# Kernel optimization log

Measured on AMD Instinct MI355X. Metric: run time of the kernel, lower is better.

Reference implementation:

```python
import jax, jax.numpy as jnp
import numpy as np

DIM = 1024
NH = 16
HD = DIM // NH  # 64
WS = 14         # window size
DFF = 4 * DIM
EPS = 1e-6


def layernorm(x, scale, bias):
    m = jnp.mean(x, axis=-1, keepdims=True)
    v = jnp.var(x, axis=-1, keepdims=True)
    return (x - m) * jax.lax.rsqrt(v + EPS) * scale + bias


def get_rel_pos(q_size, k_size, rel_pos):
    # table size (2*WS-1, HD) matches max_rel_dist, so no resize needed
    coords = (jnp.arange(q_size)[:, None] - jnp.arange(k_size)[None, :] + (k_size - 1)).astype(jnp.int32)
    return rel_pos[coords.reshape(-1)].reshape(q_size, k_size, -1)  # (q,k,HD)


def window_partition(x):
    b, h, w, c = x.shape
    pad_h = (WS - h % WS) % WS
    pad_w = (WS - w % WS) % WS
    # faithful to source: pad_w applied on axis 1, pad_h on axis 2
    x = jnp.pad(x, ((0, 0), (0, pad_w), (0, pad_h), (0, 0)))
    hp, wp = h + pad_h, w + pad_w
    x = x.reshape(b, hp // WS, WS, wp // WS, WS, c)
    windows = x.transpose(0, 1, 3, 2, 4, 5).reshape(-1, WS, WS, c)
    return windows, (hp, wp)


def window_unpartition(windows, pad_hw, hw):
    hp, wp = pad_hw
    h, w = hw
    b = windows.shape[0] // (hp * wp // WS // WS)
    x = windows.reshape(b, hp // WS, wp // WS, WS, WS, -1)
    x = x.transpose(0, 1, 3, 2, 4, 5).reshape(b, hp, wp, -1)
    return x[:, :h, :w, :]


def attention(x, qkv_kernel, qkv_bias, rel_pos_h, rel_pos_w, proj_kernel, proj_bias):
    b, h, w, _ = x.shape
    qkv = x @ qkv_kernel + qkv_bias                                  # (b,h,w,3*DIM)
    qkv = qkv.reshape(b, h * w, 3, NH, HD).transpose(2, 0, 3, 1, 4)
    qkv = qkv.reshape(3, b * NH, h * w, HD)
    q, k, v = qkv[0], qkv[1], qkv[2]
    attn = (q * HD ** -0.5) @ k.transpose(0, 2, 1)                   # (b*NH, hw, hw)
    rh = get_rel_pos(h, h, rel_pos_h)                                # (h,h,HD)
    rw = get_rel_pos(w, w, rel_pos_w)                                # (w,w,HD)
    r_q = q.reshape(-1, h, w, HD)
    rel_h = jnp.einsum('bhwc,hkc->bhwk', r_q, rh)
    rel_w = jnp.einsum('bhwc,wkc->bhwk', r_q, rw)
    attn = (attn.reshape(-1, h, w, h, w) + rel_h[:, :, :, :, None] + rel_w[:, :, :, None, :]).reshape(-1, h * w, h * w)
    attn = jax.nn.softmax(attn, axis=-1)
    out = (attn @ v).reshape(b, NH, h, w, HD).transpose(0, 2, 3, 1, 4).reshape(b, h, w, DIM)
    return out @ proj_kernel + proj_bias


def setup_inputs() -> dict:
    key = jax.random.key(0)
    ks = jax.random.split(key, 8)
    s = 0.02
    B, H, W = 4, 64, 64
    return {
        'x': jax.random.normal(ks[0], (B, H, W, DIM), jnp.float32),
        'norm1_scale': jnp.ones((DIM,), jnp.float32),
        'norm1_bias': jnp.zeros((DIM,), jnp.float32),
        'qkv_kernel': jax.random.normal(ks[1], (DIM, 3 * DIM), jnp.float32) * s,
        'qkv_bias': jnp.zeros((3 * DIM,), jnp.float32),
        'rel_pos_h': jax.random.normal(ks[2], (2 * WS - 1, HD), jnp.float32) * s,
        'rel_pos_w': jax.random.normal(ks[3], (2 * WS - 1, HD), jnp.float32) * s,
        'proj_kernel': jax.random.normal(ks[4], (DIM, DIM), jnp.float32) * s,
        'proj_bias': jnp.zeros((DIM,), jnp.float32),
        'norm2_scale': jnp.ones((DIM,), jnp.float32),
        'norm2_bias': jnp.zeros((DIM,), jnp.float32),
        'fc1_kernel': jax.random.normal(ks[5], (DIM, DFF), jnp.float32) * s,
        'fc1_bias': jnp.zeros((DFF,), jnp.float32),
        'fc2_kernel': jax.random.normal(ks[6], (DFF, DIM), jnp.float32) * s,
        'fc2_bias': jnp.zeros((DIM,), jnp.float32),
    }


def reference(x, norm1_scale, norm1_bias, qkv_kernel, qkv_bias, rel_pos_h, rel_pos_w,
              proj_kernel, proj_bias, norm2_scale, norm2_bias,
              fc1_kernel, fc1_bias, fc2_kernel, fc2_bias):
    shortcut = x
    h, w = x.shape[1], x.shape[2]
    y = layernorm(x, norm1_scale, norm1_bias)
    y, pad_hw = window_partition(y)
    y = attention(y, qkv_kernel, qkv_bias, rel_pos_h, rel_pos_w, proj_kernel, proj_bias)
    y = window_unpartition(y, pad_hw, (h, w))
    x = shortcut + y                           # drop_path=0, no layer scale
    z = layernorm(x, norm2_scale, norm2_bias)
    z = jax.nn.gelu(z @ fc1_kernel + fc1_bias, approximate=False)
    z = z @ fc2_kernel + fc2_bias
    return x + z
```

## Files before the change

kernel.cpp:

```cpp
#include <hip/hip_runtime.h>

typedef __attribute__((ext_vector_type(8))) short bf16x8;
typedef __attribute__((ext_vector_type(4))) float f32x4;
typedef __attribute__((ext_vector_type(16))) float f32x16;

__device__ __forceinline__ float b2f(ushort u) {
    union { unsigned int i; float f; } v; v.i = ((unsigned int)u) << 16; return v.f;
}
__device__ __forceinline__ ushort f2b(float f) {
    union { float f; unsigned int i; } v; v.f = f;
    unsigned int i = v.i;
    return (ushort)((i + 0x7FFFu + ((i >> 16) & 1u)) >> 16);
}
__device__ __forceinline__ void glds16(const ushort* g, ushort* l) {
    __builtin_amdgcn_global_load_lds((const __attribute__((address_space(1))) void*)g,
                                     (__attribute__((address_space(3))) void*)l, 16, 0, 0);
}
__device__ __forceinline__ void BARX() {
    asm volatile("" ::: "memory");
    __builtin_amdgcn_s_barrier();
    asm volatile("" ::: "memory");
}

__global__ __launch_bounds__(256) void ln_kernel(const float* __restrict__ x,
                                                 const float* __restrict__ sc,
                                                 const float* __restrict__ bi,
                                                 ushort* __restrict__ y) {
    __shared__ float red[8];
    long row = blockIdx.x;
    const float* xr = x + row * 1024;
    int t = threadIdx.x;
    float4 u = *(const float4*)(xr + t * 4);
    float s = u.x + u.y + u.z + u.w;
    float q = u.x * u.x + u.y * u.y + u.z * u.z + u.w * u.w;
    for (int off = 32; off > 0; off >>= 1) {
        s += __shfl_xor(s, off);
        q += __shfl_xor(q, off);
    }
    if ((t & 63) == 0) { red[t >> 6] = s; red[4 + (t >> 6)] = q; }
    __syncthreads();
    s = red[0] + red[1] + red[2] + red[3];
    q = red[4] + red[5] + red[6] + red[7];
    float mean = s * (1.0f / 1024.0f);
    float var = q * (1.0f / 1024.0f) - mean * mean;
    float rstd = rsqrtf(fmaxf(var, 0.0f) + 1e-6f);
    int c = t * 4;
    float o0 = (u.x - mean) * rstd * sc[c + 0] + bi[c + 0];
    float o1 = (u.y - mean) * rstd * sc[c + 1] + bi[c + 1];
    float o2 = (u.z - mean) * rstd * sc[c + 2] + bi[c + 2];
    float o3 = (u.w - mean) * rstd * sc[c + 3] + bi[c + 3];
    uint2 o;
    o.x = (unsigned int)f2b(o0) | ((unsigned int)f2b(o1) << 16);
    o.y = (unsigned int)f2b(o2) | ((unsigned int)f2b(o3) << 16);
    *(uint2*)(y + row * 1024 + c) = o;
}

__global__ __launch_bounds__(256) void ln_part_kernel(const float* __restrict__ x,
                                                      const float* __restrict__ sc,
                                                      const float* __restrict__ bi,
                                                      ushort* __restrict__ wy,
                                                      int win_base, int nvalid) {
    __shared__ float red[8];
    int wt = blockIdx.x;
    int lwin = wt / 196, rr = wt % 196;
    int t = threadIdx.x;
    int valid = 0;
    long xrow = 0;
    if (lwin < nvalid) {
        int gwin = win_base + lwin;
        int img = gwin / 25, wrem = gwin % 25;
        int gh = (wrem / 5) * 14 + rr / 14;
        int gw = (wrem % 5) * 14 + rr % 14;
        if (gh < 64 && gw < 64) {
            valid = 1;
            xrow = (long)img * 4096 + gh * 64 + gw;
        }
    }
    uint2 o; o.x = 0u; o.y = 0u;
    if (valid) {
        const float* xr = x + xrow * 1024;
        float4 u = *(const float4*)(xr + t * 4);
        float s = u.x + u.y + u.z + u.w;
        float q = u.x * u.x + u.y * u.y + u.z * u.z + u.w * u.w;
        for (int off = 32; off > 0; off >>= 1) {
            s += __shfl_xor(s, off);
            q += __shfl_xor(q, off);
        }
        if ((t & 63) == 0) { red[t >> 6] = s; red[4 + (t >> 6)] = q; }
        __syncthreads();
        s = red[0] + red[1] + red[2] + red[3];
        q = red[4] + red[5] + red[6] + red[7];
        float mean = s * (1.0f / 1024.0f);
        float var = q * (1.0f / 1024.0f) - mean * mean;
        float rstd = rsqrtf(fmaxf(var, 0.0f) + 1e-6f);
        int c = t * 4;
        float o0 = (u.x - mean) * rstd * sc[c + 0] + bi[c + 0];
        float o1 = (u.y - mean) * rstd * sc[c + 1] + bi[c + 1];
        float o2 = (u.z - mean) * rstd * sc[c + 2] + bi[c + 2];
        float o3 = (u.w - mean) * rstd * sc[c + 3] + bi[c + 3];
        o.x = (unsigned int)f2b(o0) | ((unsigned int)f2b(o1) << 16);
        o.y = (unsigned int)f2b(o2) | ((unsigned int)f2b(o3) << 16);
    }
    *(uint2*)(wy + (long)wt * 1024 + t * 4) = o;
}

__global__ void transpose_w(const float* __restrict__ in, ushort* __restrict__ out,
                            int K, int N) {
    __shared__ float tile[32][33];
    int n0 = blockIdx.x * 32, k0 = blockIdx.y * 32;
    int tx = threadIdx.x, ty = threadIdx.y;
    for (int i = 0; i < 32; i += 8)
        tile[ty + i][tx] = in[(long)(k0 + ty + i) * N + n0 + tx];
    __syncthreads();
    for (int i = 0; i < 32; i += 8)
        out[(long)(n0 + ty + i) * K + k0 + tx] = f2b(tile[tx][ty + i]);
}

template <int FLAGS, typename OT>
__global__ __launch_bounds__(256) void gemm_bt(const ushort* __restrict__ A,
                                               const ushort* __restrict__ Bt,
                                               const float* __restrict__ bias,
                                               const float* __restrict__ resid,
                                               OT* __restrict__ out,
                                               int M, int N, int K) {
    __shared__ __align__(16) ushort As[128 * 32];
    __shared__ __align__(16) ushort Bs[128 * 32];
    const int tid = threadIdx.x;
    const int lane = tid & 63, w = tid >> 6;
    const int wm = (w >> 1) * 64, wn = (w & 1) * 64;
    const int quad = lane >> 4, l16 = lane & 15;
    const int bm = blockIdx.x * 128, bn = blockIdx.y * 128;
    const int r = tid >> 2, kc = (tid & 3) * 8;
    f32x4 acc[4][4];
#pragma unroll
    for (int i = 0; i < 4; i++)
#pragma unroll
        for (int j = 0; j < 4; j++) acc[i][j] = (f32x4){0.f, 0.f, 0.f, 0.f};
    const ushort* Ag = A + (long)(bm + r) * K + kc;
    const ushort* Bg = Bt + (long)(bn + r) * K + kc;
    ushort* AsW = As + w * 512;
    ushort* BsW = Bs + w * 512;
    for (int k0 = 0; k0 < K; k0 += 32) {
        __syncthreads();
        glds16(Ag + k0, AsW);
        glds16(Ag + (long)64 * K + k0, AsW + 2048);
        glds16(Bg + k0, BsW);
        glds16(Bg + (long)64 * K + k0, BsW + 2048);
        __syncthreads();
        bf16x8 afr[4], bfr[4];
#pragma unroll
        for (int t = 0; t < 4; t++) {
            afr[t] = *(const bf16x8*)&As[(wm + t * 16 + l16) * 32 + quad * 8];
            bfr[t] = *(const bf16x8*)&Bs[(wn + t * 16 + l16) * 32 + quad * 8];
        }
#pragma unroll
        for (int tm = 0; tm < 4; tm++)
#pragma unroll
            for (int tn = 0; tn < 4; tn++)
                acc[tm][tn] = __builtin_amdgcn_mfma_f32_16x16x32_bf16(afr[tm], bfr[tn],
                                                                     acc[tm][tn], 0, 0, 0);
    }
#pragma unroll
    for (int tm = 0; tm < 4; tm++) {
#pragma unroll
        for (int j = 0; j < 4; j++) {
            int gm = bm + wm + tm * 16 + quad * 4 + j;
#pragma unroll
            for (int tn = 0; tn < 4; tn++) {
                int gn = bn + wn + tn * 16 + l16;
                float v = acc[tm][tn][j] + bias[gn];
                if (FLAGS & 1) v = 0.5f * v * (1.0f + erff(v * 0.70710678118654752f));
                if (FLAGS & 2) v += resid[(long)gm * N + gn];
                if (sizeof(OT) == 4) out[(long)gm * N + gn] = (OT)v;
                else out[(long)gm * N + gn] = (OT)f2b(v);
            }
        }
    }
}

#define DSR(dst, addr, imm) \
    asm volatile("ds_read_b128 %0, %1 offset:%2" : "=&v"(dst) : "v"(addr), "n"(imm));

#define MFMA32(mf, nf, a, b) \
    acc[mf][nf] = __builtin_amdgcn_mfma_f32_32x32x16_bf16(a, b, acc[mf][nf], 0, 0, 0);

#define RDK0(buf) \
    DSR(y0, b_k0, (buf) * 16384 + 0)    DSR(y1, b_k0, (buf) * 16384 + 2048) \
    DSR(x0, a_k0, (buf) * 16384 + 0)    DSR(x1, a_k0, (buf) * 16384 + 2048) \
    DSR(x2, a_k0, (buf) * 16384 + 4096) DSR(x3, a_k0, (buf) * 16384 + 6144)

#define RDK1(buf) \
    DSR(Y0, b_k1, (buf) * 16384 + 0)    DSR(Y1, b_k1, (buf) * 16384 + 2048) \
    DSR(X0, a_k1, (buf) * 16384 + 0)    DSR(X1, a_k1, (buf) * 16384 + 2048) \
    DSR(X2, a_k1, (buf) * 16384 + 4096) DSR(X3, a_k1, (buf) * 16384 + 6144)

#define MFK0 \
    MFMA32(0, 0, x0, y0) MFMA32(0, 1, x0, y1) MFMA32(1, 0, x1, y0) MFMA32(1, 1, x1, y1) \
    MFMA32(2, 0, x2, y0) MFMA32(2, 1, x2, y1) MFMA32(3, 0, x3, y0) MFMA32(3, 1, x3, y1)

#define MFK1 \
    MFMA32(0, 0, X0, Y0) MFMA32(0, 1, X0, Y1) MFMA32(1, 0, X1, Y0) MFMA32(1, 1, X1, Y1) \
    MFMA32(2, 0, X2, Y0) MFMA32(2, 1, X2, Y1) MFMA32(3, 0, X3, Y0) MFMA32(3, 1, X3, Y1)

#define LGW6 asm volatile("s_waitcnt lgkmcnt(6)" ::: "memory"); \
    __builtin_amdgcn_sched_barrier(0);

#define STAGE4(ts, dbuf) \
    glds16(Ag + (long)(ts) * 32, &As[dbuf][sdst]); \
    glds16(Ag2 + (long)(ts) * 32, &As[dbuf][sdst + 4096]); \
    glds16(Bg + (long)(ts) * 32, &Bs[dbuf][sdst]); \
    glds16(Bg2 + (long)(ts) * 32, &Bs[dbuf][sdst + 4096]);

#define TILEF(bb, ts) do {                                                               \
    STAGE4(ts + 3, ((bb) + 3) & 3)                                                       \
    __builtin_amdgcn_sched_barrier(0);                                                   \
    asm volatile("s_waitcnt vmcnt(4)" ::: "memory");                                     \
    RDK1(bb)                                                                             \
    LGW6                                                                                 \
    __builtin_amdgcn_s_setprio(1);                                                       \
    MFK0                                                                                 \
    __builtin_amdgcn_s_setprio(0);                                                       \
    __builtin_amdgcn_sched_barrier(0);                                                   \
    RDK0(((bb) + 1) & 3)                                                                 \
    LGW6                                                                                 \
    __builtin_amdgcn_s_setprio(1);                                                       \
    MFK1                                                                                 \
    __builtin_amdgcn_s_setprio(0);                                                       \
    __builtin_amdgcn_sched_barrier(0);                                                   \
    BARX();                                                                              \
} while (0)

template <int FLAGS, typename OT>
__global__ __launch_bounds__(512, 2) void gemm256(const ushort* __restrict__ A,
                                                  const ushort* __restrict__ Bt,
                                                  const float* __restrict__ bias,
                                                  const float* __restrict__ resid,
                                                  OT* __restrict__ out,
                                                  int M, int N, int K, int nbn) {
    __shared__ __align__(64) ushort As[4][8192];
    __shared__ __align__(64) ushort Bs[4][8192];
    const int nwg = gridDim.x;
    const int orig = blockIdx.x;
    const int q8 = nwg >> 3, r8 = nwg & 7;
    const int xcd = orig & 7, sub = orig >> 3;
    const int wgid = (xcd < r8 ? xcd * (q8 + 1) : r8 * (q8 + 1) + (xcd - r8) * q8) + sub;
    const int bm = (wgid / nbn) * 256, bn = (wgid % nbn) * 256;

    const int tid = threadIdx.x;
    const int lane = tid & 63, w = tid >> 6;
    const int l31 = lane & 31, hi = lane >> 5;
    const int wm = (w >> 2) * 128, wn = (w & 3) * 64;

    const int r_st = w * 16 + (lane >> 2);
    const int c_st = (((lane & 3) ^ ((lane >> 2) & 3) ^ ((lane >> 4) & 1)) << 3);
    const ushort* Ag = A + (long)(bm + r_st) * K + c_st;
    const ushort* Ag2 = Ag + (long)128 * K;
    const ushort* Bg = Bt + (long)(bn + r_st) * K + c_st;
    const ushort* Bg2 = Bg + (long)128 * K;
    const int sdst = w * 512;

    const int swz = (lane & 3) ^ ((lane >> 2) & 1);
    const int s0 = swz & 1, s1 = swz >> 1;
    const int slot_k0 = (((0 ^ s1) << 1) | (hi ^ s0)) << 4;
    const int slot_k1 = (((1 ^ s1) << 1) | (hi ^ s0)) << 4;
    const unsigned As0 =
        (unsigned)(size_t)(__attribute__((address_space(3))) ushort*)&As[0][0];
    const unsigned Bs0 =
        (unsigned)(size_t)(__attribute__((address_space(3))) ushort*)&Bs[0][0];
    const unsigned a_k0 = As0 + (unsigned)((wm + l31) * 64 + slot_k0);
    const unsigned a_k1 = As0 + (unsigned)((wm + l31) * 64 + slot_k1);
    const unsigned b_k0 = Bs0 + (unsigned)((wn + l31) * 64 + slot_k0);
    const unsigned b_k1 = Bs0 + (unsigned)((wn + l31) * 64 + slot_k1);

    f32x16 acc[4][2];
#pragma unroll
    for (int i = 0; i < 4; i++)
#pragma unroll
        for (int j = 0; j < 2; j++)
#pragma unroll
            for (int e = 0; e < 16; e++) acc[i][j][e] = 0.f;

    bf16x8 x0, x1, x2, x3, y0, y1;
    bf16x8 X0, X1, X2, X3, Y0, Y1;

    glds16(Ag, &As[0][sdst]);       glds16(Ag2, &As[0][sdst + 4096]);
    glds16(Bg, &Bs[0][sdst]);       glds16(Bg2, &Bs[0][sdst + 4096]);
    glds16(Ag + 32, &As[1][sdst]);  glds16(Ag2 + 32, &As[1][sdst + 4096]);
    glds16(Bg + 32, &Bs[1][sdst]);  glds16(Bg2 + 32, &Bs[1][sdst + 4096]);
    glds16(Ag + 64, &As[2][sdst]);  glds16(Ag2 + 64, &As[2][sdst + 4096]);
    glds16(Bg + 64, &Bs[2][sdst]);  glds16(Bg2 + 64, &Bs[2][sdst + 4096]);
    __builtin_amdgcn_sched_barrier(0);
    asm volatile("s_waitcnt vmcnt(4)" ::: "memory");
    BARX();
    RDK0(0)

    const int nt = K >> 5;
    for (int t = 0; t + 8 <= nt; t += 4) {
        TILEF(0, t);
        TILEF(1, t + 1);
        TILEF(2, t + 2);
        TILEF(3, t + 3);
    }
    TILEF(0, nt - 4);
    RDK1(1)
    LGW6
    __builtin_amdgcn_s_setprio(1); MFK0 __builtin_amdgcn_s_setprio(0);
    __builtin_amdgcn_sched_barrier(0);
    RDK0(2)
    LGW6
    __builtin_amdgcn_s_setprio(1); MFK1 __builtin_amdgcn_s_setprio(0);
    __builtin_amdgcn_sched_barrier(0);
    asm volatile("s_waitcnt vmcnt(0)" ::: "memory");
    BARX();
    RDK1(2)
    LGW6
    __builtin_amdgcn_s_setprio(1); MFK0 __builtin_amdgcn_s_setprio(0);
    __builtin_amdgcn_sched_barrier(0);
    RDK0(3)
    LGW6
    __builtin_amdgcn_s_setprio(1); MFK1 __builtin_amdgcn_s_setprio(0);
    __builtin_amdgcn_sched_barrier(0);
    RDK1(3)
    LGW6
    __builtin_amdgcn_s_setprio(1); MFK0 __builtin_amdgcn_s_setprio(0);
    __builtin_amdgcn_sched_barrier(0);
    asm volatile("s_waitcnt lgkmcnt(0)" ::: "memory");
    __builtin_amdgcn_sched_barrier(0);
    __builtin_amdgcn_s_setprio(1); MFK1 __builtin_amdgcn_s_setprio(0);
    __builtin_amdgcn_sched_barrier(0);

#pragma unroll
    for (int mf = 0; mf < 4; mf++) {
#pragma unroll
        for (int nf = 0; nf < 2; nf++) {
            const int gn = bn + wn + nf * 32 + l31;
#pragma unroll
            for (int q = 0; q < 4; q++) {
#pragma unroll
                for (int j = 0; j < 4; j++) {
                    const int gm = bm + wm + mf * 32 + q * 8 + j + 4 * hi;
                    const long ro = (long)gm * N;
                    float v = acc[mf][nf][q * 4 + j] + bias[gn];
                    if (FLAGS & 1) v = 0.5f * v * (1.0f + erff(v * 0.70710678118654752f));
                    if (FLAGS & 2) v += resid[ro + gn];
                    if (sizeof(OT) == 4) out[ro + gn] = (OT)v;
                    else out[ro + gn] = (OT)f2b(v);
                }
            }
        }
    }
}

__global__ __launch_bounds__(256) void attn_kernel(const ushort* __restrict__ qkv,
                                                   ushort* __restrict__ o_out,
                                                   const float* __restrict__ relH,
                                                   const float* __restrict__ relW,
                                                   int win0, long orow0) {
    __shared__ __align__(16) ushort Vt[64 * 200];
    __shared__ __align__(16) ushort Ps[64 * 104];
    __shared__ __align__(16) ushort sc[8 * 448];
    const int head = blockIdx.y;
    const long qbase = (long)blockIdx.x * 196 * 3072 + head * 64;
    const int gwin = win0 + blockIdx.x;
    const int img = gwin / 25, wrem = gwin % 25;
    const int whh = (wrem / 5) * 14, www = (wrem % 5) * 14;
    const int tid = threadIdx.x, lane = tid & 63, w = tid >> 6;
    const int quad = lane >> 4, l16 = lane & 15;

    for (int idx = tid; idx < 196 * 64; idx += 256) {
        int k = idx >> 6, d = idx & 63;
        Vt[d * 200 + k] = qkv[qbase + 2048 + (long)k * 3072 + d];
    }
    __syncthreads();

    bf16x8 bH[2][2], bW[2][2];
#pragma unroll
    for (int nt = 0; nt < 2; nt++) {
        int n = nt * 16 + l16;
#pragma unroll
        for (int kt = 0; kt < 2; kt++) {
            bf16x8 rh = (bf16x8){0, 0, 0, 0, 0, 0, 0, 0};
            bf16x8 rw = (bf16x8){0, 0, 0, 0, 0, 0, 0, 0};
            if (n < 27) {
                const float* ph = relH + n * 64 + kt * 32 + quad * 8;
                const float* pw = relW + n * 64 + kt * 32 + quad * 8;
#pragma unroll
                for (int e = 0; e < 8; e++) {
                    rh[e] = (short)f2b(ph[e]);
                    rw[e] = (short)f2b(pw[e]);
                }
            }
            bH[nt][kt] = rh;
            bW[nt][kt] = rw;
        }
    }

    for (int tr = w; tr < 13; tr += 4) {
        int qrow = tr * 16 + l16;
        if (qrow > 195) qrow = 195;
        bf16x8 qf0 = *(const bf16x8*)(qkv + qbase + (long)qrow * 3072 + quad * 8);
        bf16x8 qf1 = *(const bf16x8*)(qkv + qbase + (long)qrow * 3072 + 32 + quad * 8);

#pragma unroll
        for (int tab = 0; tab < 2; tab++) {
#pragma unroll
            for (int nt = 0; nt < 2; nt++) {
                f32x4 a = (f32x4){0.f, 0.f, 0.f, 0.f};
                a = __builtin_amdgcn_mfma_f32_16x16x32_bf16(qf0, tab ? bW[nt][0] : bH[nt][0],
                                                            a, 0, 0, 0);
                a = __builtin_amdgcn_mfma_f32_16x16x32_bf16(qf1, tab ? bW[nt][1] : bH[nt][1],
                                                            a, 0, 0, 0);
                int col = nt * 16 + l16;
                if (col < 27) {
#pragma unroll
                    for (int j = 0; j < 4; j++)
                        sc[(w * 2 + tab) * 448 + (quad * 4 + j) * 28 + col] = f2b(a[j]);
                }
            }
        }

        f32x4 sf[13];
#pragma unroll
        for (int tc = 0; tc < 13; tc++) {
            int krow = tc * 16 + l16;
            if (krow > 195) krow = 195;
            const ushort* kp = qkv + qbase + 1024 + (long)krow * 3072 + quad * 8;
            bf16x8 kf0 = *(const bf16x8*)kp;
            bf16x8 kf1 = *(const bf16x8*)(kp + 32);
            f32x4 s = (f32x4){0.f, 0.f, 0.f, 0.f};
            s = __builtin_amdgcn_mfma_f32_16x16x32_bf16(qf0, kf0, s, 0, 0, 0);
            s = __builtin_amdgcn_mfma_f32_16x16x32_bf16(qf1, kf1, s, 0, 0, 0);
            sf[tc] = s;
        }
#pragma unroll
        for (int tc = 0; tc < 13; tc++) {
            int c = tc * 16 + l16;
            if (c < 196) {
                int kh = c / 14, kw = c - kh * 14;
#pragma unroll
                for (int j = 0; j < 4; j++) {
                    int rr = tr * 16 + quad * 4 + j;
                    if (rr > 195) rr = 195;
                    float dh = b2f(sc[(w * 2 + 0) * 448 + (quad * 4 + j) * 28 +
                                      (rr / 14 - kh + 13)]);
                    float dw = b2f(sc[(w * 2 + 1) * 448 + (quad * 4 + j) * 28 +
                                      (rr % 14 - kw + 13)]);
                    sf[tc][j] = sf[tc][j] * 0.125f + dh + dw;
                }
            } else {
#pragma unroll
                for (int j = 0; j < 4; j++) sf[tc][j] = -30000.0f;
            }
        }
        f32x4 mx = sf[0];
#pragma unroll
        for (int tc = 1; tc < 13; tc++)
#pragma unroll
            for (int j = 0; j < 4; j++) mx[j] = fmaxf(mx[j], sf[tc][j]);
        for (int off = 1; off < 16; off <<= 1)
#pragma unroll
            for (int j = 0; j < 4; j++) mx[j] = fmaxf(mx[j], __shfl_xor(mx[j], off));
        f32x4 sum = (f32x4){0.f, 0.f, 0.f, 0.f};
#pragma unroll
        for (int tc = 0; tc < 13; tc++)
#pragma unroll
            for (int j = 0; j < 4; j++) {
                float p = __expf(sf[tc][j] - mx[j]);
                sf[tc][j] = p;
                sum[j] += p;
            }
        for (int off = 1; off < 16; off <<= 1)
#pragma unroll
            for (int j = 0; j < 4; j++) sum[j] += __shfl_xor(sum[j], off);
        f32x4 linv;
#pragma unroll
        for (int j = 0; j < 4; j++) linv[j] = 1.0f / sum[j];

        f32x4 oa[4];
#pragma unroll
        for (int tn = 0; tn < 4; tn++) oa[tn] = (f32x4){0.f, 0.f, 0.f, 0.f};
#pragma unroll
        for (int tc = 0; tc < 6; tc++) {
            int c = tc * 16 + l16;
#pragma unroll
            for (int j = 0; j < 4; j++)
                Ps[(w * 16 + quad * 4 + j) * 104 + c] = f2b(sf[tc][j]);
        }
#pragma unroll
        for (int ks = 0; ks < 3; ks++) {
            bf16x8 pf = *(const bf16x8*)&Ps[(w * 16 + l16) * 104 + ks * 32 + quad * 8];
#pragma unroll
            for (int tn = 0; tn < 4; tn++) {
                bf16x8 vf = *(const bf16x8*)&Vt[(tn * 16 + l16) * 200 + ks * 32 + quad * 8];
                oa[tn] = __builtin_amdgcn_mfma_f32_16x16x32_bf16(pf, vf, oa[tn], 0, 0, 0);
            }
        }
#pragma unroll
        for (int tc = 6; tc < 13; tc++) {
            int c = tc * 16 + l16;
            if (c < 196) {
#pragma unroll
                for (int j = 0; j < 4; j++)
                    Ps[(w * 16 + quad * 4 + j) * 104 + (c - 96)] = f2b(sf[tc][j]);
            }
        }
#pragma unroll
        for (int ks = 0; ks < 3; ks++) {
            bf16x8 pf = *(const bf16x8*)&Ps[(w * 16 + l16) * 104 + ks * 32 + quad * 8];
#pragma unroll
            for (int tn = 0; tn < 4; tn++) {
                bf16x8 vf = *(const bf16x8*)&Vt[(tn * 16 + l16) * 200 + 96 + ks * 32 + quad * 8];
                oa[tn] = __builtin_amdgcn_mfma_f32_16x16x32_bf16(pf, vf, oa[tn], 0, 0, 0);
            }
        }
        for (int kk = 192; kk < 196; kk++) {
            float pj[4];
#pragma unroll
            for (int j = 0; j < 4; j++)
                pj[j] = b2f(Ps[(w * 16 + quad * 4 + j) * 104 + 96 + (kk - 192)]);
#pragma unroll
            for (int tn = 0; tn < 4; tn++) {
                float vv = b2f(Vt[(tn * 16 + l16) * 200 + kk]);
#pragma unroll
                for (int j = 0; j < 4; j++) oa[tn][j] += pj[j] * vv;
            }
        }
#pragma unroll
        for (int j = 0; j < 4; j++) {
            int rr = tr * 16 + quad * 4 + j;
            if (rr < 196) {
                int gh = whh + rr / 14, gw = www + rr % 14;
                if (gh < 64 && gw < 64) {
                    long orow = (long)img * 4096 + gh * 64 + gw - orow0;
#pragma unroll
                    for (int tn = 0; tn < 4; tn++)
                        o_out[orow * 1024 + head * 64 + tn * 16 + l16] =
                            f2b(oa[tn][j] * linv[j]);
                }
            }
        }
    }
}

extern "C" void kernel_launch(void* const* d_in, const int* in_sizes, int n_in,
                              void* d_out, int out_size, void* d_ws, size_t ws_size,
                              hipStream_t stream) {
    const float* x = (const float*)d_in[0];
    const float* n1s = (const float*)d_in[1];
    const float* n1b = (const float*)d_in[2];
    const float* qkvW = (const float*)d_in[3];
    const float* qkvB = (const float*)d_in[4];
    const float* relH = (const float*)d_in[5];
    const float* relW = (const float*)d_in[6];
    const float* projW = (const float*)d_in[7];
    const float* projB = (const float*)d_in[8];
    const float* n2s = (const float*)d_in[9];
    const float* n2b = (const float*)d_in[10];
    const float* fc1W = (const float*)d_in[11];
    const float* fc1B = (const float*)d_in[12];
    const float* fc2W = (const float*)d_in[13];
    const float* fc2B = (const float*)d_in[14];
    float* OUT = (float*)d_out;
    char* ws = (char*)d_ws;

    if (ws_size >= 221000000ULL) {
        ushort* T0  = (ushort*)(ws);
        ushort* TP  = (ushort*)(ws + 6291456ULL);
        ushort* TF1 = (ushort*)(ws + 8388608ULL);
        ushort* TF2 = (ushort*)(ws + 16777216ULL);
        ushort* W0  = (ushort*)(ws + 25165824ULL);
        ushort* QKV = (ushort*)(ws + 65536000ULL);
        ushort* AO  = (ushort*)(ws + 186646528ULL);
        ushort* Z   = (ushort*)(ws + 25165824ULL);
        ushort* H   = (ushort*)(ws + 58720256ULL);

        transpose_w<<<dim3(96, 32), dim3(32, 8), 0, stream>>>(qkvW, T0, 1024, 3072);
        transpose_w<<<dim3(32, 32), dim3(32, 8), 0, stream>>>(projW, TP, 1024, 1024);
        transpose_w<<<dim3(128, 32), dim3(32, 8), 0, stream>>>(fc1W, TF1, 1024, 4096);
        transpose_w<<<dim3(32, 128), dim3(32, 8), 0, stream>>>(fc2W, TF2, 4096, 1024);
        ln_part_kernel<<<19712, 256, 0, stream>>>(x, n1s, n1b, W0, 0, 100);
        gemm256<0, ushort><<<924, 512, 0, stream>>>(W0, T0, qkvB, nullptr, QKV,
                                                    19712, 3072, 1024, 12);
        attn_kernel<<<dim3(100, 16), 256, 0, stream>>>(QKV, AO, relH, relW, 0, 0L);
        gemm256<2, float><<<256, 512, 0, stream>>>(AO, TP, projB, x, OUT,
                                                   16384, 1024, 1024, 4);
        ln_kernel<<<16384, 256, 0, stream>>>(OUT, n2s, n2b, Z);
        gemm256<1, ushort><<<1024, 512, 0, stream>>>(Z, TF1, fc1B, nullptr, H,
                                                     16384, 4096, 1024, 16);
        gemm256<2, float><<<256, 512, 0, stream>>>(H, TF2, fc2B, OUT, OUT,
                                                   16384, 1024, 4096, 4);
    } else if (ws_size >= 100000000ULL) {
        ushort* T0  = (ushort*)(ws);
        ushort* TP  = (ushort*)(ws + 6291456ULL);
        ushort* TF1 = (ushort*)(ws + 8388608ULL);
        ushort* TF2 = (ushort*)(ws + 16777216ULL);
        ushort* AO  = (ushort*)(ws + 25165824ULL);
        ushort* W0  = (ushort*)(ws + 58720256ULL);
        ushort* QKV = (ushort*)(ws + 68943872ULL);
        ushort* Z   = (ushort*)(ws + 25165824ULL);
        ushort* H   = (ushort*)(ws + 58720256ULL);

        transpose_w<<<dim3(96, 32), dim3(32, 8), 0, stream>>>(qkvW, T0, 1024, 3072);
        transpose_w<<<dim3(32, 32), dim3(32, 8), 0, stream>>>(projW, TP, 1024, 1024);
        transpose_w<<<dim3(128, 32), dim3(32, 8), 0, stream>>>(fc1W, TF1, 1024, 4096);
        transpose_w<<<dim3(32, 128), dim3(32, 8), 0, stream>>>(fc2W, TF2, 4096, 1024);
        for (int i = 0; i < 4; i++) {
            ln_part_kernel<<<4992, 256, 0, stream>>>(x, n1s, n1b, W0, i * 25, 25);
            gemm_bt<0, ushort><<<dim3(39, 24), 256, 0, stream>>>(W0, T0, qkvB, nullptr,
                                                                 QKV, 4992, 3072, 1024);
            attn_kernel<<<dim3(25, 16), 256, 0, stream>>>(QKV, AO, relH, relW, i * 25, 0L);
        }
        gemm_bt<2, float><<<dim3(128, 8), 256, 0, stream>>>(AO, TP, projB, x, OUT,
                                                            16384, 1024, 1024);
        for (int c = 0; c < 4; c++) {
            float* xc = OUT + (long)c * 4194304;
            ln_kernel<<<4096, 256, 0, stream>>>(xc, n2s, n2b, Z);
            gemm_bt<1, ushort><<<dim3(32, 32), 256, 0, stream>>>(Z, TF1, fc1B, nullptr, H,
                                                                 4096, 4096, 1024);
            gemm_bt<2, float><<<dim3(32, 8), 256, 0, stream>>>(H, TF2, fc2B, xc, xc,
                                                               4096, 1024, 4096);
        }
    } else {
        ushort* T0 = (ushort*)(ws);
        ushort* W0 = (ushort*)(ws + 6291456ULL);
        ushort* W1 = (ushort*)(ws + 16515072ULL);
        ushort* W2 = (ushort*)(ws + 22806528ULL);
        ushort* F1 = (ushort*)(ws);
        ushort* F2 = (ushort*)(ws + 8388608ULL);
        ushort* Z  = (ushort*)(ws + 16777216ULL);
        ushort* H  = (ushort*)(ws + 18874368ULL);

        transpose_w<<<dim3(96, 32), dim3(32, 8), 0, stream>>>(qkvW, T0, 1024, 3072);
        for (int i = 0; i < 4; i++) {
            const float* xi = x + (long)i * 4194304;
            ln_part_kernel<<<4992, 256, 0, stream>>>(x, n1s, n1b, W0, i * 25, 25);
            for (int g = 0; g < 5; g++) {
                gemm_bt<0, ushort><<<dim3(8, 24), 256, 0, stream>>>(
                    W0 + (long)g * 980 * 1024, T0, qkvB, nullptr, W1, 1024, 3072, 1024);
                attn_kernel<<<dim3(5, 16), 256, 0, stream>>>(W1, W2, relH, relW,
                                                             i * 25 + g * 5, (long)i * 4096);
            }
            transpose_w<<<dim3(32, 32), dim3(32, 8), 0, stream>>>(projW, W1, 1024, 1024);
            gemm_bt<2, float><<<dim3(32, 8), 256, 0, stream>>>(
                W2, W1, projB, xi, OUT + (long)i * 4194304, 4096, 1024, 1024);
        }
        transpose_w<<<dim3(128, 32), dim3(32, 8), 0, stream>>>(fc1W, F1, 1024, 4096);
        transpose_w<<<dim3(32, 128), dim3(32, 8), 0, stream>>>(fc2W, F2, 4096, 1024);
        for (int c = 0; c < 16; c++) {
            float* xc = OUT + (long)c * 1048576;
            ln_kernel<<<1024, 256, 0, stream>>>(xc, n2s, n2b, Z);
            gemm_bt<1, ushort><<<dim3(8, 32), 256, 0, stream>>>(Z, F1, fc1B, nullptr, H,
                                                                1024, 4096, 1024);
            gemm_bt<2, float><<<dim3(8, 8), 256, 0, stream>>>(H, F2, fc2B, xc, xc,
                                                              1024, 1024, 4096);
        }
    }
}
```

Before: 909.3 us.

## Load GEMM A operand directly from global into registers, staging only B in LDS

The 256x256 bf16 GEMM kernel stops staging the A tile through shared memory. Each wave now loads its own A fragments straight from global memory into double-buffered registers one k-step ahead, while B stays in a 4-stage LDS ring, now filled with a different per-wave row mapping. This halves LDS traffic and capacity per block and removes the A ds_reads. In exchange it raises VGPR pressure, and because the two waves sharing an M half both read the same A rows, global and L2 traffic for A doubles, with less latency hiding for those loads.

```diff
diff --git a/kernel.cpp b/kernel.cpp
--- a/kernel.cpp
+++ b/kernel.cpp
@@ -185,46 +185,51 @@
     acc[mf][nf] = __builtin_amdgcn_mfma_f32_32x32x16_bf16(a, b, acc[mf][nf], 0, 0, 0);
 
 #define RDK0(buf) \
-    DSR(y0, b_k0, (buf) * 16384 + 0)    DSR(y1, b_k0, (buf) * 16384 + 2048) \
-    DSR(x0, a_k0, (buf) * 16384 + 0)    DSR(x1, a_k0, (buf) * 16384 + 2048) \
-    DSR(x2, a_k0, (buf) * 16384 + 4096) DSR(x3, a_k0, (buf) * 16384 + 6144)
-
+    DSR(y0, b_k0, (buf) * 16384 + 0)    DSR(y1, b_k0, (buf) * 16384 + 2048)
 #define RDK1(buf) \
-    DSR(Y0, b_k1, (buf) * 16384 + 0)    DSR(Y1, b_k1, (buf) * 16384 + 2048) \
-    DSR(X0, a_k1, (buf) * 16384 + 0)    DSR(X1, a_k1, (buf) * 16384 + 2048) \
-    DSR(X2, a_k1, (buf) * 16384 + 4096) DSR(X3, a_k1, (buf) * 16384 + 6144)
-
-#define MFK0 \
-    MFMA32(0, 0, x0, y0) MFMA32(0, 1, x0, y1) MFMA32(1, 0, x1, y0) MFMA32(1, 1, x1, y1) \
-    MFMA32(2, 0, x2, y0) MFMA32(2, 1, x2, y1) MFMA32(3, 0, x3, y0) MFMA32(3, 1, x3, y1)
-
-#define MFK1 \
-    MFMA32(0, 0, X0, Y0) MFMA32(0, 1, X0, Y1) MFMA32(1, 0, X1, Y0) MFMA32(1, 1, X1, Y1) \
-    MFMA32(2, 0, X2, Y0) MFMA32(2, 1, X2, Y1) MFMA32(3, 0, X3, Y0) MFMA32(3, 1, X3, Y1)
-
-#define LGW6 asm volatile("s_waitcnt lgkmcnt(6)" ::: "memory"); \
-    __builtin_amdgcn_sched_barrier(0);
-
-#define STAGE4(ts, dbuf) \
-    glds16(Ag + (long)(ts) * 32, &As[dbuf][sdst]); \
-    glds16(Ag2 + (long)(ts) * 32, &As[dbuf][sdst + 4096]); \
-    glds16(Bg + (long)(ts) * 32, &Bs[dbuf][sdst]); \
-    glds16(Bg2 + (long)(ts) * 32, &Bs[dbuf][sdst + 4096]);
-
-#define TILEF(bb, ts) do {                                                               \
-    STAGE4(ts + 3, ((bb) + 3) & 3)                                                       \
+    DSR(Y0, b_k1, (buf) * 16384 + 0)    DSR(Y1, b_k1, (buf) * 16384 + 2048)
+
+#define MFK0(S) \
+    MFMA32(0, 0, S##0, y0) MFMA32(0, 1, S##0, y1) MFMA32(1, 0, S##1, y0) MFMA32(1, 1, S##1, y1) \
+    MFMA32(2, 0, S##2, y0) MFMA32(2, 1, S##2, y1) MFMA32(3, 0, S##3, y0) MFMA32(3, 1, S##3, y1)
+#define MFK1(S) \
+    MFMA32(0, 0, S##4, Y0) MFMA32(0, 1, S##4, Y1) MFMA32(1, 0, S##5, Y0) MFMA32(1, 1, S##5, Y1) \
+    MFMA32(2, 0, S##6, Y0) MFMA32(2, 1, S##6, Y1) MFMA32(3, 0, S##7, Y0) MFMA32(3, 1, S##7, Y1)
+
+#define LGW2 asm volatile("s_waitcnt lgkmcnt(2)" ::: "memory"); \
+    __builtin_amdgcn_sched_barrier(0);
+#define LGW0 asm volatile("s_waitcnt lgkmcnt(0)" ::: "memory"); \
+    __builtin_amdgcn_sched_barrier(0);
+
+#define ALOAD(S, ts) \
+    S##0 = *(const bf16x8*)(Ar0 + (ts) * 32);      \
+    S##1 = *(const bf16x8*)(Ar1 + (ts) * 32);      \
+    S##2 = *(const bf16x8*)(Ar2 + (ts) * 32);      \
+    S##3 = *(const bf16x8*)(Ar3 + (ts) * 32);      \
+    S##4 = *(const bf16x8*)(Ar0 + (ts) * 32 + 16); \
+    S##5 = *(const bf16x8*)(Ar1 + (ts) * 32 + 16); \
+    S##6 = *(const bf16x8*)(Ar2 + (ts) * 32 + 16); \
+    S##7 = *(const bf16x8*)(Ar3 + (ts) * 32 + 16);
+
+#define STAGE_B(ts, dbuf) \
+    glds16(Bg0 + (long)(ts) * 32, &Bs[dbuf][w * 1024]); \
+    glds16(Bg1 + (long)(ts) * 32, &Bs[dbuf][w * 1024 + 512]);
+
+#define TILEX(bb, ts, CUR, NXT) do {                                                     \
+    STAGE_B(ts + 3, ((bb) + 3) & 3)                                                      \
+    ALOAD(NXT, ts + 1)                                                                   \
     __builtin_amdgcn_sched_barrier(0);                                                   \
-    asm volatile("s_waitcnt vmcnt(4)" ::: "memory");                                     \
+    asm volatile("s_waitcnt vmcnt(10)" ::: "memory");                                    \
     RDK1(bb)                                                                             \
-    LGW6                                                                                 \
+    LGW2                                                                                 \
     __builtin_amdgcn_s_setprio(1);                                                       \
-    MFK0                                                                                 \
+    MFK0(CUR)                                                                            \
     __builtin_amdgcn_s_setprio(0);                                                       \
     __builtin_amdgcn_sched_barrier(0);                                                   \
     RDK0(((bb) + 1) & 3)                                                                 \
-    LGW6                                                                                 \
+    LGW2                                                                                 \
     __builtin_amdgcn_s_setprio(1);                                                       \
-    MFK1                                                                                 \
+    MFK1(CUR)                                                                            \
     __builtin_amdgcn_s_setprio(0);                                                       \
     __builtin_amdgcn_sched_barrier(0);                                                   \
     BARX();                                                                              \
@@ -237,7 +242,6 @@
                                                   const float* __restrict__ resid,
                                                   OT* __restrict__ out,
                                                   int M, int N, int K, int nbn) {
-    __shared__ __align__(64) ushort As[4][8192];
     __shared__ __align__(64) ushort Bs[4][8192];
     const int nwg = gridDim.x;
     const int orig = blockIdx.x;
@@ -251,24 +255,21 @@
     const int l31 = lane & 31, hi = lane >> 5;
     const int wm = (w >> 2) * 128, wn = (w & 3) * 64;
 
-    const int r_st = w * 16 + (lane >> 2);
     const int c_st = (((lane & 3) ^ ((lane >> 2) & 3) ^ ((lane >> 4) & 1)) << 3);
-    const ushort* Ag = A + (long)(bm + r_st) * K + c_st;
-    const ushort* Ag2 = Ag + (long)128 * K;
-    const ushort* Bg = Bt + (long)(bn + r_st) * K + c_st;
-    const ushort* Bg2 = Bg + (long)128 * K;
-    const int sdst = w * 512;
+    const ushort* Bg0 = Bt + (long)(bn + w * 32 + (lane >> 2)) * K + c_st;
+    const ushort* Bg1 = Bg0 + (long)16 * K;
+
+    const ushort* Ar0 = A + (long)(bm + wm + l31) * K + hi * 8;
+    const ushort* Ar1 = Ar0 + (long)32 * K;
+    const ushort* Ar2 = Ar0 + (long)64 * K;
+    const ushort* Ar3 = Ar0 + (long)96 * K;
 
     const int swz = (lane & 3) ^ ((lane >> 2) & 1);
     const int s0 = swz & 1, s1 = swz >> 1;
     const int slot_k0 = (((0 ^ s1) << 1) | (hi ^ s0)) << 4;
     const int slot_k1 = (((1 ^ s1) << 1) | (hi ^ s0)) << 4;
-    const unsigned As0 =
-        (unsigned)(size_t)(__attribute__((address_space(3))) ushort*)&As[0][0];
     const unsigned Bs0 =
         (unsigned)(size_t)(__attribute__((address_space(3))) ushort*)&Bs[0][0];
-    const unsigned a_k0 = As0 + (unsigned)((wm + l31) * 64 + slot_k0);
-    const unsigned a_k1 = As0 + (unsigned)((wm + l31) * 64 + slot_k1);
     const unsigned b_k0 = Bs0 + (unsigned)((wn + l31) * 64 + slot_k0);
     const unsigned b_k1 = Bs0 + (unsigned)((wn + l31) * 64 + slot_k1);
 
@@ -280,53 +281,58 @@
 #pragma unroll
             for (int e = 0; e < 16; e++) acc[i][j][e] = 0.f;
 
-    bf16x8 x0, x1, x2, x3, y0, y1;
-    bf16x8 X0, X1, X2, X3, Y0, Y1;
-
-    glds16(Ag, &As[0][sdst]);       glds16(Ag2, &As[0][sdst + 4096]);
-    glds16(Bg, &Bs[0][sdst]);       glds16(Bg2, &Bs[0][sdst + 4096]);
-    glds16(Ag + 32, &As[1][sdst]);  glds16(Ag2 + 32, &As[1][sdst + 4096]);
-    glds16(Bg + 32, &Bs[1][sdst]);  glds16(Bg2 + 32, &Bs[1][sdst + 4096]);
-    glds16(Ag + 64, &As[2][sdst]);  glds16(Ag2 + 64, &As[2][sdst + 4096]);
-    glds16(Bg + 64, &Bs[2][sdst]);  glds16(Bg2 + 64, &Bs[2][sdst + 4096]);
-    __builtin_amdgcn_sched_barrier(0);
-    asm volatile("s_waitcnt vmcnt(4)" ::: "memory");
+    bf16x8 P0, P1, P2, P3, P4, P5, P6, P7;
+    bf16x8 Q0, Q1, Q2, Q3, Q4, Q5, Q6, Q7;
+    bf16x8 y0, y1, Y0, Y1;
+
+    STAGE_B(0, 0)
+    STAGE_B(1, 1)
+    STAGE_B(2, 2)
+    ALOAD(P, 0)
+    __builtin_amdgcn_sched_barrier(0);
+    asm volatile("s_waitcnt vmcnt(10)" ::: "memory");
     BARX();
     RDK0(0)
 
     const int nt = K >> 5;
     for (int t = 0; t + 8 <= nt; t += 4) {
-        TILEF(0, t);
-        TILEF(1, t + 1);
-        TILEF(2, t + 2);
-        TILEF(3, t + 3);
-    }
-    TILEF(0, nt - 4);
+        TILEX(0, t, P, Q);
+        TILEX(1, t + 1, Q, P);
+        TILEX(2, t + 2, P, Q);
+        TILEX(3, t + 3, Q, P);
+    }
+    TILEX(0, nt - 4, P, Q);
+    ALOAD(P, nt - 2)
+    __builtin_amdgcn_sched_barrier(0);
+    asm volatile("s_waitcnt vmcnt(8)" ::: "memory");
     RDK1(1)
-    LGW6
-    __builtin_amdgcn_s_setprio(1); MFK0 __builtin_amdgcn_s_setprio(0);
+    LGW2
+    __builtin_amdgcn_s_setprio(1); MFK0(Q) __builtin_amdgcn_s_setprio(0);
     __builtin_amdgcn_sched_barrier(0);
     RDK0(2)
-    LGW6
-    __builtin_amdgcn_s_setprio(1); MFK1 __builtin_amdgcn_s_setprio(0);
-    __builtin_amdgcn_sched_barrier(0);
+    LGW2
+    __builtin_amdgcn_s_setprio(1); MFK1(Q) __builtin_amdgcn_s_setprio(0);
+    __builtin_amdgcn_sched_barrier(0);
+    BARX();
+    ALOAD(Q, nt - 1)
+    __builtin_amdgcn_sched_barrier(0);
+    asm volatile("s_waitcnt vmcnt(8)" ::: "memory");
+    RDK1(2)
+    LGW2
+    __builtin_amdgcn_s_setprio(1); MFK0(P) __builtin_amdgcn_s_setprio(0);
+    __builtin_amdgcn_sched_barrier(0);
+    RDK0(3)
+    LGW2
+    __builtin_amdgcn_s_setprio(1); MFK1(P) __builtin_amdgcn_s_setprio(0);
+    __builtin_amdgcn_sched_barrier(0);
+    BARX();
     asm volatile("s_waitcnt vmcnt(0)" ::: "memory");
-    BARX();
-    RDK1(2)
-    LGW6
-    __builtin_amdgcn_s_setprio(1); MFK0 __builtin_amdgcn_s_setprio(0);
-    __builtin_amdgcn_sched_barrier(0);
-    RDK0(3)
-    LGW6
-    __builtin_amdgcn_s_setprio(1); MFK1 __builtin_amdgcn_s_setprio(0);
-    __builtin_amdgcn_sched_barrier(0);
     RDK1(3)
-    LGW6
-    __builtin_amdgcn_s_setprio(1); MFK0 __builtin_amdgcn_s_setprio(0);
-    __builtin_amdgcn_sched_barrier(0);
-    asm volatile("s_waitcnt lgkmcnt(0)" ::: "memory");
-    __builtin_amdgcn_sched_barrier(0);
-    __builtin_amdgcn_s_setprio(1); MFK1 __builtin_amdgcn_s_setprio(0);
+    LGW2
+    __builtin_amdgcn_s_setprio(1); MFK0(Q) __builtin_amdgcn_s_setprio(0);
+    __builtin_amdgcn_sched_barrier(0);
+    LGW0
+    __builtin_amdgcn_s_setprio(1); MFK1(Q) __builtin_amdgcn_s_setprio(0);
     __builtin_amdgcn_sched_barrier(0);
 
 #pragma unroll
```

After: 1.429 ms. 1.57x slower.
